# Performance work log

Hardware: AMD Instinct MI355X
Metric: run time of the kernel (lower is better)

## Reference

```python
import jax, jax.numpy as jnp
import numpy as np
import math

N_SPIXELS = 256
N_ITER = 5
TAU = 0.01
R = 1          # candidate_radius
NORMALIZE = True


def _unfold(x, kh, kw, ph, pw, sh, sw):
    """torch.nn.functional.unfold, returning (b, c, kh, kw, oh, ow)."""
    b, c, H, W = x.shape
    xp = jnp.pad(x, ((0, 0), (0, 0), (ph, ph), (pw, pw)))
    oh = (H + 2 * ph - kh) // sh + 1
    ow = (W + 2 * pw - kw) // sw + 1
    rows = jnp.arange(oh)[:, None] * sh + jnp.arange(kh)[None, :]   # (oh, kh)
    cols = jnp.arange(ow)[:, None] * sw + jnp.arange(kw)[None, :]   # (ow, kw)
    p = xp[:, :, rows][:, :, :, :, cols]    # (b, c, oh, kh, ow, kw)
    return p.transpose(0, 1, 3, 5, 2, 4)    # (b, c, kh, kw, oh, ow)


def _l2norm(t):
    return t / jnp.linalg.norm(t, axis=1, keepdims=True)


def _forward(x):
    b, c, H, W = x.shape
    hs = int(math.sqrt(N_SPIXELS * H / W))
    ws = int(math.sqrt(N_SPIXELS * W / H))
    sh = (H + hs - 1) // hs
    sw = (W + ws - 1) // ws
    # adaptive_avg_pool2d: H, W chosen divisible by hs, ws -> exact block mean
    clst = x.reshape(b, c, hs, H // hs, ws, W // ws).mean(axis=(3, 5))
    if NORMALIZE:
        x = _l2norm(x)
        clst = _l2norm(clst)
    # pad to multiple of (hs, ws): zero for the chosen shapes
    nr = 2 * R + 1
    s2p = None
    for _ in range(N_ITER):
        # update_clst_feats: overlapping unfold over (3*sh, 3*sw) window
        up = _unfold(x, sh * nr, sw * nr, sh * R, sw * R, sh, sw)    # (b,c,3sh,3sw,hs,ws)
        up = up.reshape(b, c, sh * nr * sw * nr, hs, ws)
        sim = jnp.einsum('bcphw,bchw->bphw', up, clst)
        sim = jnp.where(sim == 0, -jnp.inf, sim)                     # mask padded pixels
        s2p = jax.nn.softmax(sim / TAU, axis=1)
        clst = jnp.einsum('bphw,bcphw->bchw', s2p, up)
        if NORMALIZE:
            clst = _l2norm(clst)
    # compute_elem_to_center_assignment
    cand = _unfold(clst, nr, nr, R, R, 1, 1).reshape(b, c, nr * nr, hs * ws)
    # non-overlapping unfold of x with kernel == stride: pure reshape
    uef = x.reshape(b, c, hs, sh, ws, sw).transpose(0, 1, 3, 5, 2, 4)
    uef = uef.reshape(b, c, sh * sw, hs * ws)
    sim = jnp.einsum('bkcn,bkpn->bcpn', cand, uef)   # (b, nr^2, sh*sw, hs*ws)
    # non-overlapping fold back to (H, W)
    sim = sim.reshape(b, nr * nr, sh, sw, hs, ws).transpose(0, 1, 4, 2, 5, 3)
    sim = sim.reshape(b, nr * nr, H, W)
    sim = jnp.where(sim == 0, -jnp.inf, sim)         # mask padded candidate clusters
    p2s = jax.nn.softmax(sim / TAU, axis=1)
    return clst, p2s, s2p


def setup_inputs() -> dict:
    key = jax.random.key(0)
    x = jax.random.normal(key, (2, 32, 256, 256), dtype=jnp.float32)
    return {"x": x}


def reference(x):
    return _forward(x)
```

## Files before the change

kernel.cpp:

```cpp
#include <hip/hip_runtime.h>
#include <math.h>

#define TAU_INV 100.0f
#define SHIFTED_EXP(s) expf(((s) - 0.5f) * TAU_INV)

__device__ inline float combine_one(const float* __restrict__ Sin,
                                    const float* __restrict__ dpin,
                                    int b, int ti, int tj, int c) {
    float acc = 0.f, den = 0.f;
    if (ti >= 0 && ti < 16 && tj >= 0 && tj < 16) {
#pragma unroll
        for (int u = 0; u < 9; ++u) {
            int oy = u / 3 - 1, ox = u % 3 - 1;
            int ii = ti + oy, jj = tj + ox;
            if (ii >= 0 && ii < 16 && jj >= 0 && jj < 16) {
                int src = ((b * 256 + ii * 16 + jj) * 9) + (1 - oy) * 3 + (1 - ox);
                acc += Sin[(size_t)src * 32 + c];
                den += dpin[src];
            }
        }
    }
    float mean = (den > 0.f) ? acc / den : 0.f;
    float p = mean * mean;
#pragma unroll
    for (int k = 16; k >= 1; k >>= 1) p += __shfl_xor(p, k);
    return (p > 0.f) ? mean * (1.0f / sqrtf(p)) : 0.f;
}

__global__ __launch_bounds__(256) void prep_init_kernel(const float* __restrict__ x,
                                                        float* __restrict__ xn,
                                                        float* __restrict__ clst0) {
    int blk = blockIdx.x;
    int b = blk >> 8;
    int cell = blk & 255;
    int ci = cell >> 4, cj = cell & 15;
    int t = threadIdx.x;
    int py = t >> 4, px = t & 15;
    int y = ci * 16 + py, xx = cj * 16 + px;
    int rem = y * 256 + xx;

    __shared__ float sraw[256 * 33];
    __shared__ float red[256];

    const float* xb = x + (size_t)b * (32 * 65536);
    float v[32];
    float ss = 0.f;
#pragma unroll
    for (int c = 0; c < 32; ++c) {
        float tv = xb[c * 65536 + rem];
        v[c] = tv;
        ss += tv * tv;
        sraw[t * 33 + c] = tv;
    }
    float rn = 1.0f / sqrtf(ss);
    float4* outp = (float4*)(xn + ((size_t)b * 65536 + rem) * 32);
#pragma unroll
    for (int q = 0; q < 8; ++q)
        outp[q] = make_float4(v[4*q]*rn, v[4*q+1]*rn, v[4*q+2]*rn, v[4*q+3]*rn);

    __syncthreads();
    int c = t & 31, pg = t >> 5;
    float acc = 0.f;
#pragma unroll
    for (int k = 0; k < 32; ++k) acc += sraw[(pg * 32 + k) * 33 + c];
    red[t] = acc;
    __syncthreads();
    if (t < 128) red[t] += red[t + 128];
    __syncthreads();
    if (t < 64) red[t] += red[t + 64];
    __syncthreads();
    if (t < 32) {
        float m = (red[t] + red[t + 32]) * (1.0f / 256.0f);
        float p = m * m;
#pragma unroll
        for (int k = 16; k >= 1; k >>= 1) p += __shfl_xor(p, k);
        clst0[(size_t)blk * 32 + t] = m * (1.0f / sqrtf(p));
    }
}

__global__ __launch_bounds__(256) void accum9c_kernel(const float* __restrict__ xn,
                                                      const float* __restrict__ clst0,
                                                      const float* __restrict__ Sin,
                                                      const float* __restrict__ dpin,
                                                      float* __restrict__ Sout,
                                                      float* __restrict__ dpout,
                                                      float* __restrict__ clstin5,
                                                      int it) {
    int blk = blockIdx.x;
    int b = blk >> 8;
    int cell = blk & 255;
    int bi = cell >> 4, bj = cell & 15;
    int t = threadIdx.x;

    __shared__ float sx[256 * 33];
    __shared__ float sclst[9][32];
    __shared__ float se[9][256];
    __shared__ float sacc[8][9][32];
    __shared__ float sdw[4][9];

    if (it == 0) {
        for (int u = t; u < 288; u += 256) {
            int q = u >> 5, c = u & 31;
            int ii = bi + q / 3 - 1, jj = bj + q % 3 - 1;
            float v = 0.f;
            if (ii >= 0 && ii < 16 && jj >= 0 && jj < 16)
                v = clst0[((size_t)(b * 256 + ii * 16 + jj)) * 32 + c];
            sclst[q][c] = v;
        }
    } else {
        {
            int q = t >> 5, c = t & 31;
            float v = combine_one(Sin, dpin, b, bi + q / 3 - 1, bj + q % 3 - 1, c);
            sclst[q][c] = v;
            if (it == 4 && q == 4)
                clstin5[(size_t)blk * 32 + c] = v;
        }
        if (t < 32)
            sclst[8][t] = combine_one(Sin, dpin, b, bi + 1, bj + 1, t);
    }

    int y = bi * 16 + (t >> 4), xx = bj * 16 + (t & 15);
    const float4* f4 = (const float4*)(xn + ((size_t)(b * 65536 + y * 256 + xx)) * 32);
    float fv[32];
#pragma unroll
    for (int q = 0; q < 8; ++q) {
        float4 v = f4[q];
        fv[4*q] = v.x; fv[4*q+1] = v.y; fv[4*q+2] = v.z; fv[4*q+3] = v.w;
    }
#pragma unroll
    for (int c = 0; c < 32; ++c) sx[t * 33 + c] = fv[c];
    __syncthreads();

    int wid = t >> 6, lane = t & 63;
#pragma unroll
    for (int q = 0; q < 9; ++q) {
        float s = 0.f;
#pragma unroll
        for (int c = 0; c < 32; ++c) s += fv[c] * sclst[q][c];
        float ev = (s == 0.f) ? 0.f : SHIFTED_EXP(s);
        se[q][t] = ev;
        float d = ev;
#pragma unroll
        for (int k = 32; k >= 1; k >>= 1) d += __shfl_xor(d, k);
        if (lane == 0) sdw[wid][q] = d;
    }
    __syncthreads();
    if (t < 9) dpout[blk * 9 + t] = sdw[0][t] + sdw[1][t] + sdw[2][t] + sdw[3][t];

    {
        int c = t & 31, pg = t >> 5;
        float acc[9];
#pragma unroll
        for (int q = 0; q < 9; ++q) acc[q] = 0.f;
#pragma unroll
        for (int k = 0; k < 32; ++k) {
            int p = pg * 32 + k;
            float xv = sx[p * 33 + c];
#pragma unroll
            for (int q = 0; q < 9; ++q) acc[q] = fmaf(se[q][p], xv, acc[q]);
        }
#pragma unroll
        for (int q = 0; q < 9; ++q) sacc[pg][q][c] = acc[q];
    }
    __syncthreads();

    {
        int q = t >> 5, cc = t & 31;
        float s8 = 0.f;
#pragma unroll
        for (int g = 0; g < 8; ++g) s8 += sacc[g][q][cc];
        Sout[((size_t)blk * 9 + q) * 32 + cc] = s8;
        if (t < 32) {
            float s9 = 0.f;
#pragma unroll
            for (int g = 0; g < 8; ++g) s9 += sacc[g][8][t];
            Sout[((size_t)blk * 9 + 8) * 32 + t] = s9;
        }
    }
}

__global__ __launch_bounds__(256) void tail_kernel(const float* __restrict__ xn,
                                                   const float* __restrict__ Sin,
                                                   const float* __restrict__ dpin,
                                                   const float* __restrict__ clstin5,
                                                   float* __restrict__ out_clst,
                                                   float* __restrict__ out_p2s,
                                                   float* __restrict__ out_s2p) {
    int blk = blockIdx.x;
    int b = blk >> 8;
    int cell = blk & 255;
    int ky0 = cell >> 4, kx0 = cell & 15;
    int t = threadIdx.x;

    __shared__ float sx[256 * 33];
    __shared__ float L[256 * 33];
    __shared__ float sclst[9][32];
    __shared__ float srd[256];

    {
        int q = t >> 5, c = t & 31;
        float v = combine_one(Sin, dpin, b, ky0 + q / 3 - 1, kx0 + q % 3 - 1, c);
        sclst[q][c] = v;
        if (q == 4)
            out_clst[((size_t)b * 32 + c) * 256 + cell] = v;
    }
    if (t < 32)
        sclst[8][t] = combine_one(Sin, dpin, b, ky0 + 1, kx0 + 1, t);

    for (int u = t; u < 8192; u += 256)
        sx[(u >> 5) * 33 + (u & 31)] = clstin5[(size_t)b * 8192 + u];

    {
        int r = t >> 4, s = t & 15;
        const float4* f4 = (const float4*)(xn +
            ((size_t)(b * 65536 + (16 * r + ky0) * 256 + 16 * s + kx0)) * 32);
#pragma unroll
        for (int q = 0; q < 8; ++q) {
            float4 v = f4[q];
            L[t * 33 + 4*q]     = v.x;
            L[t * 33 + 4*q + 1] = v.y;
            L[t * 33 + 4*q + 2] = v.z;
            L[t * 33 + 4*q + 3] = v.w;
        }
    }

    {
        int i = t >> 4, j = t & 15;
        float den = 0.f;
#pragma unroll
        for (int u = 0; u < 9; ++u) {
            int oy = u / 3 - 1, ox = u % 3 - 1;
            int ii = i + oy, jj = j + ox;
            if (ii >= 0 && ii < 16 && jj >= 0 && jj < 16)
                den += dpin[((b * 256 + ii * 16 + jj) * 9) + (1 - oy) * 3 + (1 - ox)];
        }
        srd[t] = 1.0f / den;
    }
    __syncthreads();

    {
        int i = t >> 4, j = t & 15;
        const float* cl = sx + t * 33;
        float rd = srd[t];
#pragma unroll
        for (int a = 0; a < 3; ++a) {
#pragma unroll
            for (int bb = 0; bb < 3; ++bb) {
                int r = i + a - 1, s2 = j + bb - 1;
                float val = 0.f;
                if (r >= 0 && r < 16 && s2 >= 0 && s2 < 16) {
                    const float* f = L + (r * 16 + s2) * 33;
                    float s = 0.f;
#pragma unroll
                    for (int c = 0; c < 32; ++c) s += f[c] * cl[c];
                    if (s != 0.f) val = SHIFTED_EXP(s) * rd;
                }
                int p = (ky0 + 16 * a) * 48 + kx0 + 16 * bb;
                out_s2p[(size_t)(b * 2304 + p) * 256 + t] = val;
            }
        }
    }

    {
        int py = t >> 4, px = t & 15;
        int rem = (ky0 * 16 + py) * 256 + kx0 * 16 + px;
        const float4* f4 = (const float4*)(xn + ((size_t)b * 65536 + rem) * 32);
        float fv[32];
#pragma unroll
        for (int q = 0; q < 8; ++q) {
            float4 v = f4[q];
            fv[4*q] = v.x; fv[4*q+1] = v.y; fv[4*q+2] = v.z; fv[4*q+3] = v.w;
        }
        float l[9];
        float mx = -INFINITY;
#pragma unroll
        for (int q = 0; q < 9; ++q) {
            float s = 0.f;
#pragma unroll
            for (int c = 0; c < 32; ++c) s += fv[c] * sclst[q][c];
            l[q] = (s == 0.f) ? -INFINITY : s * TAU_INV;
            mx = fmaxf(mx, l[q]);
        }
        float e[9], sum = 0.f;
#pragma unroll
        for (int q = 0; q < 9; ++q) {
            e[q] = (l[q] == -INFINITY) ? 0.f : expf(l[q] - mx);
            sum += e[q];
        }
        float rs = 1.0f / sum;
#pragma unroll
        for (int q = 0; q < 9; ++q)
            out_p2s[((size_t)b * 9 + q) * 65536 + rem] = e[q] * rs;
    }
}

extern "C" void kernel_launch(void* const* d_in, const int* in_sizes, int n_in,
                              void* d_out, int out_size, void* d_ws, size_t ws_size,
                              hipStream_t stream) {
    const float* x = (const float*)d_in[0];
    float* out = (float*)d_out;

    float* out_clst = out;
    float* out_p2s  = out + 16384;
    float* out_s2p  = out + 16384 + 1179648;

    float* ws = (float*)d_ws;
    float* xn      = ws;
    float* clst0   = xn + 4194304;
    float* Sa      = clst0 + 16384;
    float* Sb      = Sa + 147456;
    float* dpa     = Sb + 147456;
    float* dpb     = dpa + 4608;
    float* clstin5 = dpb + 4608;

    prep_init_kernel<<<512, 256, 0, stream>>>(x, xn, clst0);

    float* Sin = Sa;  float* dpin = dpa;
    float* Sout = Sb; float* dpout = dpb;
    for (int it = 0; it < 5; ++it) {
        accum9c_kernel<<<512, 256, 0, stream>>>(xn, clst0, Sin, dpin,
                                                Sout, dpout, clstin5, it);
        float* ts = Sin; Sin = Sout; Sout = ts;
        float* td = dpin; dpin = dpout; dpout = td;
    }
    tail_kernel<<<512, 256, 0, stream>>>(xn, Sin, dpin, clstin5,
                                         out_clst, out_p2s, out_s2p);
}
```

Measured before the change: 101.8 us.

## Double block size to 512 threads, splitting per-pixel work across thread halves

```diff
diff --git a/kernel.cpp b/kernel.cpp
--- a/kernel.cpp
+++ b/kernel.cpp
@@ -27,43 +27,51 @@
     return (p > 0.f) ? mean * (1.0f / sqrtf(p)) : 0.f;
 }
 
-__global__ __launch_bounds__(256) void prep_init_kernel(const float* __restrict__ x,
-                                                        float* __restrict__ xn,
-                                                        float* __restrict__ clst0) {
+__global__ __launch_bounds__(512, 4) void prep_init_kernel(const float* __restrict__ x,
+                                                           float* __restrict__ xn,
+                                                           float* __restrict__ clst0) {
     int blk = blockIdx.x;
     int b = blk >> 8;
     int cell = blk & 255;
     int ci = cell >> 4, cj = cell & 15;
     int t = threadIdx.x;
-    int py = t >> 4, px = t & 15;
-    int y = ci * 16 + py, xx = cj * 16 + px;
-    int rem = y * 256 + xx;
+    int p = t & 255, h = t >> 8;
+    int py = p >> 4, px = p & 15;
+    int rem = (ci * 16 + py) * 256 + cj * 16 + px;
 
     __shared__ float sraw[256 * 33];
-    __shared__ float red[256];
+    __shared__ float ssh[512];
+    __shared__ float red[512];
 
     const float* xb = x + (size_t)b * (32 * 65536);
-    float v[32];
-    float ss = 0.f;
-#pragma unroll
-    for (int c = 0; c < 32; ++c) {
+    float v[16];
+    float ssp = 0.f;
+#pragma unroll
+    for (int k = 0; k < 16; ++k) {
+        int c = h * 16 + k;
         float tv = xb[c * 65536 + rem];
-        v[c] = tv;
-        ss += tv * tv;
-        sraw[t * 33 + c] = tv;
-    }
-    float rn = 1.0f / sqrtf(ss);
-    float4* outp = (float4*)(xn + ((size_t)b * 65536 + rem) * 32);
-#pragma unroll
-    for (int q = 0; q < 8; ++q)
-        outp[q] = make_float4(v[4*q]*rn, v[4*q+1]*rn, v[4*q+2]*rn, v[4*q+3]*rn);
-
-    __syncthreads();
-    int c = t & 31, pg = t >> 5;
-    float acc = 0.f;
-#pragma unroll
-    for (int k = 0; k < 32; ++k) acc += sraw[(pg * 32 + k) * 33 + c];
-    red[t] = acc;
+        v[k] = tv;
+        ssp += tv * tv;
+        sraw[p * 33 + c] = tv;
+    }
+    ssh[t] = ssp;
+    __syncthreads();
+    float rn = 1.0f / sqrtf(ssh[p] + ssh[p + 256]);
+    {
+        float4* outp = (float4*)(xn + ((size_t)b * 65536 + rem) * 32 + h * 16);
+#pragma unroll
+        for (int q = 0; q < 4; ++q)
+            outp[q] = make_float4(v[4*q]*rn, v[4*q+1]*rn, v[4*q+2]*rn, v[4*q+3]*rn);
+    }
+    {
+        int c = t & 31, pg = t >> 5;
+        float acc = 0.f;
+#pragma unroll
+        for (int k = 0; k < 16; ++k) acc += sraw[(pg * 16 + k) * 33 + c];
+        red[t] = acc;
+    }
+    __syncthreads();
+    if (t < 256) red[t] += red[t + 256];
     __syncthreads();
     if (t < 128) red[t] += red[t + 128];
     __syncthreads();
@@ -71,21 +79,21 @@
     __syncthreads();
     if (t < 32) {
         float m = (red[t] + red[t + 32]) * (1.0f / 256.0f);
-        float p = m * m;
-#pragma unroll
-        for (int k = 16; k >= 1; k >>= 1) p += __shfl_xor(p, k);
-        clst0[(size_t)blk * 32 + t] = m * (1.0f / sqrtf(p));
-    }
-}
-
-__global__ __launch_bounds__(256) void accum9c_kernel(const float* __restrict__ xn,
-                                                      const float* __restrict__ clst0,
-                                                      const float* __restrict__ Sin,
-                                                      const float* __restrict__ dpin,
-                                                      float* __restrict__ Sout,
-                                                      float* __restrict__ dpout,
-                                                      float* __restrict__ clstin5,
-                                                      int it) {
+        float pp = m * m;
+#pragma unroll
+        for (int k = 16; k >= 1; k >>= 1) pp += __shfl_xor(pp, k);
+        clst0[(size_t)blk * 32 + t] = m * (1.0f / sqrtf(pp));
+    }
+}
+
+__global__ __launch_bounds__(512, 4) void accum9c_kernel(const float* __restrict__ xn,
+                                                         const float* __restrict__ clst0,
+                                                         const float* __restrict__ Sin,
+                                                         const float* __restrict__ dpin,
+                                                         float* __restrict__ Sout,
+                                                         float* __restrict__ dpout,
+                                                         float* __restrict__ clstin5,
+                                                         int it) {
     int blk = blockIdx.x;
     int b = blk >> 8;
     int cell = blk & 255;
@@ -93,14 +101,14 @@
     int t = threadIdx.x;
 
     __shared__ float sx[256 * 33];
+    __shared__ float se[9 * 256];
+    __shared__ float sacc[16 * 9 * 32];
     __shared__ float sclst[9][32];
-    __shared__ float se[9][256];
-    __shared__ float sacc[8][9][32];
-    __shared__ float sdw[4][9];
+    __shared__ float sdw[8][9];
 
     if (it == 0) {
-        for (int u = t; u < 288; u += 256) {
-            int q = u >> 5, c = u & 31;
+        if (t < 288) {
+            int q = t >> 5, c = t & 31;
             int ii = bi + q / 3 - 1, jj = bj + q % 3 - 1;
             float v = 0.f;
             if (ii >= 0 && ii < 16 && jj >= 0 && jj < 16)
@@ -108,18 +116,18 @@
             sclst[q][c] = v;
         }
     } else {
-        {
+        if (t < 288) {
             int q = t >> 5, c = t & 31;
             float v = combine_one(Sin, dpin, b, bi + q / 3 - 1, bj + q % 3 - 1, c);
             sclst[q][c] = v;
             if (it == 4 && q == 4)
                 clstin5[(size_t)blk * 32 + c] = v;
         }
-        if (t < 32)
-            sclst[8][t] = combine_one(Sin, dpin, b, bi + 1, bj + 1, t);
-    }
-
-    int y = bi * 16 + (t >> 4), xx = bj * 16 + (t & 15);
+    }
+    __syncthreads();
+
+    int p = t & 255, h = t >> 8;
+    int y = bi * 16 + (p >> 4), xx = bj * 16 + (p & 15);
     const float4* f4 = (const float4*)(xn + ((size_t)(b * 65536 + y * 256 + xx)) * 32);
     float fv[32];
 #pragma unroll
@@ -127,25 +135,44 @@
         float4 v = f4[q];
         fv[4*q] = v.x; fv[4*q+1] = v.y; fv[4*q+2] = v.z; fv[4*q+3] = v.w;
     }
-#pragma unroll
-    for (int c = 0; c < 32; ++c) sx[t * 33 + c] = fv[c];
-    __syncthreads();
+    if (h == 0) {
+#pragma unroll
+        for (int c = 0; c < 32; ++c) sx[p * 33 + c] = fv[c];
+    }
 
     int wid = t >> 6, lane = t & 63;
-#pragma unroll
-    for (int q = 0; q < 9; ++q) {
-        float s = 0.f;
-#pragma unroll
-        for (int c = 0; c < 32; ++c) s += fv[c] * sclst[q][c];
-        float ev = (s == 0.f) ? 0.f : SHIFTED_EXP(s);
-        se[q][t] = ev;
-        float d = ev;
-#pragma unroll
-        for (int k = 32; k >= 1; k >>= 1) d += __shfl_xor(d, k);
-        if (lane == 0) sdw[wid][q] = d;
-    }
-    __syncthreads();
-    if (t < 9) dpout[blk * 9 + t] = sdw[0][t] + sdw[1][t] + sdw[2][t] + sdw[3][t];
+    if (h == 0) {
+#pragma unroll
+        for (int q = 0; q < 4; ++q) {
+            float s = 0.f;
+#pragma unroll
+            for (int c = 0; c < 32; ++c) s += fv[c] * sclst[q][c];
+            float ev = (s == 0.f) ? 0.f : SHIFTED_EXP(s);
+            se[q * 256 + p] = ev;
+            float d = ev;
+#pragma unroll
+            for (int k = 32; k >= 1; k >>= 1) d += __shfl_xor(d, k);
+            if (lane == 0) sdw[wid][q] = d;
+        }
+    } else {
+#pragma unroll
+        for (int q = 4; q < 9; ++q) {
+            float s = 0.f;
+#pragma unroll
+            for (int c = 0; c < 32; ++c) s += fv[c] * sclst[q][c];
+            float ev = (s == 0.f) ? 0.f : SHIFTED_EXP(s);
+            se[q * 256 + p] = ev;
+            float d = ev;
+#pragma unroll
+            for (int k = 32; k >= 1; k >>= 1) d += __shfl_xor(d, k);
+            if (lane == 0) sdw[wid][q] = d;
+        }
+    }
+    __syncthreads();
+    if (t < 9) {
+        int w0 = (t < 4) ? 0 : 4;
+        dpout[blk * 9 + t] = sdw[w0][t] + sdw[w0+1][t] + sdw[w0+2][t] + sdw[w0+3][t];
+    }
 
     {
         int c = t & 31, pg = t >> 5;
@@ -153,78 +180,70 @@
 #pragma unroll
         for (int q = 0; q < 9; ++q) acc[q] = 0.f;
 #pragma unroll
-        for (int k = 0; k < 32; ++k) {
-            int p = pg * 32 + k;
-            float xv = sx[p * 33 + c];
-#pragma unroll
-            for (int q = 0; q < 9; ++q) acc[q] = fmaf(se[q][p], xv, acc[q]);
-        }
-#pragma unroll
-        for (int q = 0; q < 9; ++q) sacc[pg][q][c] = acc[q];
-    }
-    __syncthreads();
-
-    {
+        for (int k = 0; k < 16; ++k) {
+            int pp = pg * 16 + k;
+            float xv = sx[pp * 33 + c];
+#pragma unroll
+            for (int q = 0; q < 9; ++q) acc[q] = fmaf(se[q * 256 + pp], xv, acc[q]);
+        }
+#pragma unroll
+        for (int q = 0; q < 9; ++q) sacc[(pg * 9 + q) * 32 + c] = acc[q];
+    }
+    __syncthreads();
+    if (t < 288) {
         int q = t >> 5, cc = t & 31;
-        float s8 = 0.f;
-#pragma unroll
-        for (int g = 0; g < 8; ++g) s8 += sacc[g][q][cc];
-        Sout[((size_t)blk * 9 + q) * 32 + cc] = s8;
-        if (t < 32) {
-            float s9 = 0.f;
-#pragma unroll
-            for (int g = 0; g < 8; ++g) s9 += sacc[g][8][t];
-            Sout[((size_t)blk * 9 + 8) * 32 + t] = s9;
-        }
-    }
-}
-
-__global__ __launch_bounds__(256) void tail_kernel(const float* __restrict__ xn,
-                                                   const float* __restrict__ Sin,
-                                                   const float* __restrict__ dpin,
-                                                   const float* __restrict__ clstin5,
-                                                   float* __restrict__ out_clst,
-                                                   float* __restrict__ out_p2s,
-                                                   float* __restrict__ out_s2p) {
+        float s = 0.f;
+#pragma unroll
+        for (int g = 0; g < 16; ++g) s += sacc[(g * 9 + q) * 32 + cc];
+        Sout[((size_t)blk * 9 + q) * 32 + cc] = s;
+    }
+}
+
+__global__ __launch_bounds__(512, 4) void tail_kernel(const float* __restrict__ xn,
+                                                      const float* __restrict__ Sin,
+                                                      const float* __restrict__ dpin,
+                                                      const float* __restrict__ clstin5,
+                                                      float* __restrict__ out_clst,
+                                                      float* __restrict__ out_p2s,
+                                                      float* __restrict__ out_s2p) {
     int blk = blockIdx.x;
     int b = blk >> 8;
     int cell = blk & 255;
     int ky0 = cell >> 4, kx0 = cell & 15;
     int t = threadIdx.x;
 
-    __shared__ float sx[256 * 33];
-    __shared__ float L[256 * 33];
+    __shared__ float bufA[256 * 33];
+    __shared__ float bufB[256 * 33];
     __shared__ float sclst[9][32];
     __shared__ float srd[256];
 
-    {
+    if (t < 288) {
         int q = t >> 5, c = t & 31;
         float v = combine_one(Sin, dpin, b, ky0 + q / 3 - 1, kx0 + q % 3 - 1, c);
         sclst[q][c] = v;
         if (q == 4)
             out_clst[((size_t)b * 32 + c) * 256 + cell] = v;
     }
-    if (t < 32)
-        sclst[8][t] = combine_one(Sin, dpin, b, ky0 + 1, kx0 + 1, t);
-
-    for (int u = t; u < 8192; u += 256)
-        sx[(u >> 5) * 33 + (u & 31)] = clstin5[(size_t)b * 8192 + u];
+
+    for (int u = t; u < 8192; u += 512)
+        bufA[(u >> 5) * 33 + (u & 31)] = clstin5[(size_t)b * 8192 + u];
 
     {
-        int r = t >> 4, s = t & 15;
+        int p = t & 255, h = t >> 8;
+        int r = p >> 4, s = p & 15;
         const float4* f4 = (const float4*)(xn +
-            ((size_t)(b * 65536 + (16 * r + ky0) * 256 + 16 * s + kx0)) * 32);
-#pragma unroll
-        for (int q = 0; q < 8; ++q) {
+            ((size_t)(b * 65536 + (16 * r + ky0) * 256 + 16 * s + kx0)) * 32 + h * 16);
+#pragma unroll
+        for (int q = 0; q < 4; ++q) {
             float4 v = f4[q];
-            L[t * 33 + 4*q]     = v.x;
-            L[t * 33 + 4*q + 1] = v.y;
-            L[t * 33 + 4*q + 2] = v.z;
-            L[t * 33 + 4*q + 3] = v.w;
-        }
-    }
-
-    {
+            bufB[p * 33 + h * 16 + 4*q]     = v.x;
+            bufB[p * 33 + h * 16 + 4*q + 1] = v.y;
+            bufB[p * 33 + h * 16 + 4*q + 2] = v.z;
+            bufB[p * 33 + h * 16 + 4*q + 3] = v.w;
+        }
+    }
+
+    if (t < 256) {
         int i = t >> 4, j = t & 15;
         float den = 0.f;
 #pragma unroll
@@ -238,9 +257,9 @@
     }
     __syncthreads();
 
-    {
+    if (t < 256) {
         int i = t >> 4, j = t & 15;
-        const float* cl = sx + t * 33;
+        const float* cl = bufA + t * 33;
         float rd = srd[t];
 #pragma unroll
         for (int a = 0; a < 3; ++a) {
@@ -249,7 +268,7 @@
                 int r = i + a - 1, s2 = j + bb - 1;
                 float val = 0.f;
                 if (r >= 0 && r < 16 && s2 >= 0 && s2 < 16) {
-                    const float* f = L + (r * 16 + s2) * 33;
+                    const float* f = bufB + (r * 16 + s2) * 33;
                     float s = 0.f;
 #pragma unroll
                     for (int c = 0; c < 32; ++c) s += f[c] * cl[c];
@@ -259,10 +278,9 @@
                 out_s2p[(size_t)(b * 2304 + p) * 256 + t] = val;
             }
         }
-    }
-
-    {
-        int py = t >> 4, px = t & 15;
+    } else {
+        int p = t - 256;
+        int py = p >> 4, px = p & 15;
         int rem = (ky0 * 16 + py) * 256 + kx0 * 16 + px;
         const float4* f4 = (const float4*)(xn + ((size_t)b * 65536 + rem) * 32);
         float fv[32];
@@ -313,16 +331,16 @@
     float* dpb     = dpa + 4608;
     float* clstin5 = dpb + 4608;
 
-    prep_init_kernel<<<512, 256, 0, stream>>>(x, xn, clst0);
+    prep_init_kernel<<<512, 512, 0, stream>>>(x, xn, clst0);
 
     float* Sin = Sa;  float* dpin = dpa;
     float* Sout = Sb; float* dpout = dpb;
     for (int it = 0; it < 5; ++it) {
-        accum9c_kernel<<<512, 256, 0, stream>>>(xn, clst0, Sin, dpin,
+        accum9c_kernel<<<512, 512, 0, stream>>>(xn, clst0, Sin, dpin,
                                                 Sout, dpout, clstin5, it);
         float* ts = Sin; Sin = Sout; Sout = ts;
         float* td = dpin; dpin = dpout; dpout = td;
     }
-    tail_kernel<<<512, 256, 0, stream>>>(xn, Sin, dpin, clstin5,
+    tail_kernel<<<512, 512, 0, stream>>>(xn, Sin, dpin, clstin5,
                                          out_clst, out_p2s, out_s2p);
 }
```

Result: faster. 94.87 us, median of 2 (-6.8%).
